# Kernel tuning notes

Hardware: AMD Instinct MI355X
Metric: run time of the kernel (lower is better)

The kernel has to match this reference:

```python
import jax, jax.numpy as jnp
import numpy as np

N = 4096          # number_of_node
DIN = 3           # dim_input (forced: fc1 expects N*dim_input == N*3 after last stage)
DOUT = 4          # dim_output
DACT = N          # dim_action defaults to number_of_node
B = 128


def setup_inputs() -> dict:
    key = jax.random.key(0)
    ks = jax.random.split(key, 12)
    X = jax.random.normal(ks[0], (B, N * DIN), dtype=jnp.float32)
    adj = jax.random.uniform(ks[1], (N, N), dtype=jnp.float32)
    def lin(kw, kb, fan_in, fan_out):
        bound = 1.0 / np.sqrt(fan_in)
        W = jax.random.uniform(kw, (fan_in, fan_out), minval=-bound, maxval=bound, dtype=jnp.float32)
        b = jax.random.uniform(kb, (fan_out,), minval=-bound, maxval=bound, dtype=jnp.float32)
        return W, b
    W1, b1 = lin(ks[2], ks[3], DIN, 4)
    W2, b2 = lin(ks[4], ks[5], 4, DOUT)
    W3, b3 = lin(ks[6], ks[7], DOUT, 3)
    Wfc, bfc = lin(ks[8], ks[9], N * DIN, 54)
    Wout, bout = lin(ks[10], ks[11], 54, DACT)
    return {"X": X, "adj": adj, "W1": W1, "b1": b1, "W2": W2, "b2": b2,
            "W3": W3, "b3": b3, "Wfc": Wfc, "bfc": bfc, "Wout": Wout, "bout": bout}


def reference(X, adj, W1, b1, W2, b2, W3, b3, Wfc, bfc, Wout, bout):
    # X: [B, N*DIN] -> [B, N, DIN]
    h = X.reshape(X.shape[0], N, DIN)
    # three (adj @ h) aggregations fused with tiny Linear + ReLU
    h = jax.nn.relu(jnp.einsum('nm,bmf->bnf', adj, h) @ W1 + b1)   # [B,N,4]
    h = jax.nn.relu(jnp.einsum('nm,bmf->bnf', adj, h) @ W2 + b2)   # [B,N,DOUT]
    h = jax.nn.relu(jnp.einsum('nm,bmf->bnf', adj, h) @ W3 + b3)   # [B,N,3]
    flat = h.reshape(h.shape[0], -1)                               # [B, N*3]
    hid = jax.nn.relu(flat @ Wfc + bfc)                            # [B, 54]
    q_value = hid @ Wout + bout                                    # [B, DACT]
    return q_value
```

## Files before the change

### kernel.cpp

```cpp
#include <hip/hip_runtime.h>


typedef __bf16 bf16x8 __attribute__((ext_vector_type(8)));
typedef float  f32x4  __attribute__((ext_vector_type(4)));

#define N_NODE 4096
#define BATCH  128

__global__ __launch_bounds__(256) void prep_k(const float* __restrict__ adj,
                                              __bf16* __restrict__ adjB,
                                              const float* __restrict__ X,
                                              const float* __restrict__ W1,
                                              __bf16* __restrict__ G0,
                                              float* __restrict__ hid_acc) {
    const int blk = blockIdx.x, tx = threadIdx.x;
    if (blk < 8192) {
        const int g = blk * 256 + tx;
        const int lane = g & 63, ka = (g >> 6) & 127, rb = g >> 13;
        const int row = rb * 16 + (lane & 15);
        const int kb  = ka * 32 + ((lane >> 4) & 3) * 8;
        const float4* s = (const float4*)(adj + (size_t)row * 4096 + kb);
        float4 u = s[0];
        float4 v = s[1];
        bf16x8 o = { (__bf16)u.x, (__bf16)u.y, (__bf16)u.z, (__bf16)u.w,
                     (__bf16)v.x, (__bf16)v.y, (__bf16)v.z, (__bf16)v.w };
        *(bf16x8*)(adjB + (size_t)g * 8) = o;
    } else if (blk < 9216) {
        const int g = (blk - 8192) * 256 + tx;
        const int lp = g & 63, cbg = (g >> 6) & 31, kc = g >> 11;
        const int c = cbg * 16 + (lp & 15);
        const int b = c >> 2, f = c & 3;
        const float w0 = W1[0 * 4 + f], w1 = W1[1 * 4 + f], w2 = W1[2 * 4 + f];
        const int mb = kc * 32 + ((lp >> 4) & 3) * 8;
        const float* Xb = X + (size_t)b * 12288 + (size_t)mb * 3;
        bf16x8 o;
#pragma unroll
        for (int j = 0; j < 8; ++j) {
            const float v = Xb[j * 3 + 0] * w0 + Xb[j * 3 + 1] * w1 + Xb[j * 3 + 2] * w2;
            o[j] = (__bf16)v;
        }
        *(bf16x8*)(G0 + (size_t)g * 8) = o;
    } else {
        const int i = (blk - 9216) * 256 + tx;
        if (i < BATCH * 54) hid_acc[i] = 0.f;
    }
}

template <int MODE>
__global__ __launch_bounds__(512, 4) void gcn_k(const __bf16* __restrict__ A,
                                                const __bf16* __restrict__ Bp,
                                                const float* __restrict__ Wa,
                                                const float* __restrict__ ba,
                                                const float* __restrict__ Wb,
                                                __bf16* __restrict__ Op,
                                                float* __restrict__ hidOut) {
    __shared__ __align__(16) unsigned char smem[49664];
    const int tx = threadIdx.x;
    const int wave = tx >> 6, lane = tx & 63;
    const int quad = lane >> 4, lr = lane & 15;

    const int l = blockIdx.x;
    const int xcd = l & 7, s = l >> 3;
    const int mi = xcd * 8 + (s & 7), ci = s >> 3;
    const int m0 = mi * 64;

    const __bf16* pA[4];
#pragma unroll
    for (int i = 0; i < 4; ++i)
        pA[i] = A + (size_t)(mi * 4 + i) * 65536 + wave * 512 + lane * 8;
    const __bf16* pB[4];
#pragma unroll
    for (int j = 0; j < 4; ++j)
        pB[j] = Bp + (size_t)(wave * 32 + (ci * 4 + j)) * 512 + lane * 8;

    f32x4 acc[4][4] = {};

#pragma unroll 4
    for (int kt = 0; kt < 16; ++kt) {
        bf16x8 af[4], bv[4];
#pragma unroll
        for (int i = 0; i < 4; ++i)
            af[i] = *(const bf16x8*)(pA[i] + kt * 4096);
#pragma unroll
        for (int j = 0; j < 4; ++j)
            bv[j] = *(const bf16x8*)(pB[j] + kt * 131072);
#pragma unroll
        for (int i = 0; i < 4; ++i)
#pragma unroll
            for (int j = 0; j < 4; ++j)
                acc[i][j] = __builtin_amdgcn_mfma_f32_16x16x32_bf16(
                    af[i], bv[j], acc[i][j], 0, 0, 0);
    }

    float* part = (float*)smem;
    float* Ct   = (float*)(smem + 32768);
#pragma unroll
    for (int r = 0; r < 4; ++r) {
        __syncthreads();
#pragma unroll
        for (int u = 0; u < 4; ++u)
            *(f32x4*)(part + (wave * 4 + u) * 256 + lane * 4) = acc[r][u];
        __syncthreads();
        if (wave < 4) {
            f32x4 fin = {};
#pragma unroll
            for (int sl = 0; sl < 8; ++sl)
                fin += *(const f32x4*)(part + (sl * 4 + wave) * 256 + lane * 4);
#pragma unroll
            for (int rr = 0; rr < 4; ++rr)
                Ct[(r * 16 + quad * 4 + rr) * 66 + wave * 16 + lr] = fin[rr];
        }
    }
    __syncthreads();

    if (MODE == 0) {
        const int g2 = tx;
        const int lp = g2 & 63, cbl = (g2 >> 6) & 3, kcl = g2 >> 8;
        const int cl = cbl * 16 + (lp & 15);
        const float bf = ba[cl & 3];
        const int mb = kcl * 32 + ((lp >> 4) & 3) * 8;
        bf16x8 o;
#pragma unroll
        for (int j = 0; j < 8; ++j)
            o[j] = (__bf16)fmaxf(Ct[(mb + j) * 66 + cl] + bf, 0.f);
        *(bf16x8*)(Op + ((size_t)((mi * 2 + kcl) * 32 + (ci * 4 + cbl)) * 64 + lp) * 8) = o;
    } else if (MODE == 1) {
        float W2l[16], W3l[12], bl2[4];
#pragma unroll
        for (int i = 0; i < 16; ++i) W2l[i] = Wa[i];
#pragma unroll
        for (int i = 0; i < 12; ++i) W3l[i] = Wb[i];
#pragma unroll
        for (int i = 0; i < 4; ++i) bl2[i] = ba[i];
        const int g2 = tx;
        const int lp = g2 & 63, cbl = (g2 >> 6) & 3, kcl = g2 >> 8;
        const int cl = cbl * 16 + (lp & 15);
        const int bloc = cl >> 2, f3 = cl & 3;
        const int mb = kcl * 32 + ((lp >> 4) & 3) * 8;
        bf16x8 o;
#pragma unroll
        for (int j = 0; j < 8; ++j) {
            const float* row = &Ct[(mb + j) * 66 + bloc * 4];
            float v = 0.f;
            if (f3 < 3) {
#pragma unroll
                for (int fo = 0; fo < 4; ++fo) {
                    const float tmp = fmaxf(row[0] * W2l[fo] + row[1] * W2l[4 + fo] +
                                            row[2] * W2l[8 + fo] + row[3] * W2l[12 + fo] +
                                            bl2[fo], 0.f);
                    const float w3a = W3l[fo * 3 + 0], w3b = W3l[fo * 3 + 1],
                                w3c = W3l[fo * 3 + 2];
                    v += tmp * (f3 == 0 ? w3a : (f3 == 1 ? w3b : w3c));
                }
            }
            o[j] = (__bf16)v;
        }
        *(bf16x8*)(Op + ((size_t)((mi * 2 + kcl) * 32 + (ci * 4 + cbl)) * 64 + lp) * 8) = o;
    } else {
        float* red = part;
        const float b30 = ba[0], b31 = ba[1], b32 = ba[2];
        float accf[16];
#pragma unroll
        for (int b = 0; b < 16; ++b) accf[b] = 0.f;
        if (lane < 54) {
            for (int nn = 0; nn < 8; ++nn) {
                const int n = wave * 8 + nn;
#pragma unroll
                for (int f = 0; f < 3; ++f) {
                    const float w = Wa[((size_t)(m0 + n) * 3 + f) * 54 + lane];
                    const float bf = (f == 0) ? b30 : (f == 1 ? b31 : b32);
#pragma unroll
                    for (int b = 0; b < 16; ++b) {
                        const float r = fmaxf(Ct[n * 66 + b * 4 + f] + bf, 0.f);
                        accf[b] += r * w;
                    }
                }
            }
        }
#pragma unroll
        for (int b = 0; b < 16; ++b)
            red[(wave * 16 + b) * 64 + lane] = accf[b];
        __syncthreads();
        if (wave == 0 && lane < 54) {
            for (int b = 0; b < 16; ++b) {
                float s2 = 0.f;
#pragma unroll
                for (int w8 = 0; w8 < 8; ++w8)
                    s2 += red[(w8 * 16 + b) * 64 + lane];
                atomicAdd(&hidOut[(ci * 16 + b) * 54 + lane], s2);
            }
        }
    }
}

__global__ __launch_bounds__(256) void fc2_k(const float* __restrict__ hid_acc,
                                             const float* __restrict__ bfc,
                                             const float* __restrict__ Wout,
                                             const float* __restrict__ bout,
                                             float* __restrict__ out) {
    const int tx = threadIdx.x;
    const int a  = blockIdx.x * 256 + tx;
    const int b0 = blockIdx.y * 4;
    __shared__ float hs[4 * 54];
    if (tx < 216) {
        const int j = tx % 54;
        hs[tx] = fmaxf(hid_acc[b0 * 54 + tx] + bfc[j], 0.f);
    }
    __syncthreads();
    float a0 = 0.f, a1 = 0.f, a2 = 0.f, a3 = 0.f;
    for (int j = 0; j < 54; ++j) {
        float w = Wout[(size_t)j * N_NODE + a];
        a0 += hs[0 * 54 + j] * w;
        a1 += hs[1 * 54 + j] * w;
        a2 += hs[2 * 54 + j] * w;
        a3 += hs[3 * 54 + j] * w;
    }
    float bo = bout[a];
    out[(size_t)(b0 + 0) * N_NODE + a] = a0 + bo;
    out[(size_t)(b0 + 1) * N_NODE + a] = a1 + bo;
    out[(size_t)(b0 + 2) * N_NODE + a] = a2 + bo;
    out[(size_t)(b0 + 3) * N_NODE + a] = a3 + bo;
}

extern "C" void kernel_launch(void* const* d_in, const int* in_sizes, int n_in,
                              void* d_out, int out_size, void* d_ws, size_t ws_size,
                              hipStream_t stream) {
    const float* X    = (const float*)d_in[0];
    const float* adj  = (const float*)d_in[1];
    const float* W1   = (const float*)d_in[2];
    const float* b1   = (const float*)d_in[3];
    const float* W2   = (const float*)d_in[4];
    const float* b2   = (const float*)d_in[5];
    const float* W3   = (const float*)d_in[6];
    const float* b3   = (const float*)d_in[7];
    const float* Wfc  = (const float*)d_in[8];
    const float* bfc  = (const float*)d_in[9];
    const float* Wout = (const float*)d_in[10];
    const float* bout = (const float*)d_in[11];
    float* out = (float*)d_out;

    char* w = (char*)d_ws;
    __bf16* adjB = (__bf16*)w;
    __bf16* G0   = (__bf16*)(w + 33554432);
    __bf16* H1   = (__bf16*)(w + 33554432 + 4194304);
    __bf16* H2g  = (__bf16*)(w + 33554432 + 2 * 4194304);
    float*  hid  = (float*)(w + 33554432 + 3 * 4194304);

    prep_k<<<9243, 256, 0, stream>>>(adj, adjB, X, W1, G0, hid);

    gcn_k<0><<<512, 512, 0, stream>>>(adjB, G0, nullptr, b1, nullptr, H1, nullptr);
    gcn_k<1><<<512, 512, 0, stream>>>(adjB, H1, W2, b2, W3, H2g, nullptr);
    gcn_k<2><<<512, 512, 0, stream>>>(adjB, H2g, Wfc, b3, nullptr, nullptr, hid);

    fc2_k<<<dim3(16, 32), 256, 0, stream>>>(hid, bfc, Wout, bout, out);
}
```

Measured before the change: 209.2 us.

## Double GCN block row tile to 128 with 1024-thread blocks

Each gcn block now covers 128 adjacency rows using 16 waves: two row groups of eight K-split waves each, with the launch reduced to 256 blocks. The split-K reduction and the per-mode epilogue run in two serialized halves over the same shared buffer. For MODE 2, the partial FC sums of the two row groups are merged in shared memory before the atomic add. The aim is more reuse of the B operand per block and fewer blocks. In exchange it adds extra barriers, leaves half the waves idle during the epilogues, and `launch_bounds(1024,4)` may push the compiler toward tight register limits.

```diff
diff --git a/kernel.cpp b/kernel.cpp
--- a/kernel.cpp
+++ b/kernel.cpp
@@ -47,31 +47,32 @@
 }
 
 template <int MODE>
-__global__ __launch_bounds__(512, 4) void gcn_k(const __bf16* __restrict__ A,
-                                                const __bf16* __restrict__ Bp,
-                                                const float* __restrict__ Wa,
-                                                const float* __restrict__ ba,
-                                                const float* __restrict__ Wb,
-                                                __bf16* __restrict__ Op,
-                                                float* __restrict__ hidOut) {
+__global__ __launch_bounds__(1024, 4) void gcn_k(const __bf16* __restrict__ A,
+                                                 const __bf16* __restrict__ Bp,
+                                                 const float* __restrict__ Wa,
+                                                 const float* __restrict__ ba,
+                                                 const float* __restrict__ Wb,
+                                                 __bf16* __restrict__ Op,
+                                                 float* __restrict__ hidOut) {
     __shared__ __align__(16) unsigned char smem[49664];
     const int tx = threadIdx.x;
     const int wave = tx >> 6, lane = tx & 63;
+    const int wm = wave >> 3, wk = wave & 7;
     const int quad = lane >> 4, lr = lane & 15;
 
     const int l = blockIdx.x;
     const int xcd = l & 7, s = l >> 3;
-    const int mi = xcd * 8 + (s & 7), ci = s >> 3;
-    const int m0 = mi * 64;
+    const int mi = xcd * 4 + (s & 3), ci = s >> 2;
+    const int m0 = mi * 128;
 
     const __bf16* pA[4];
 #pragma unroll
     for (int i = 0; i < 4; ++i)
-        pA[i] = A + (size_t)(mi * 4 + i) * 65536 + wave * 512 + lane * 8;
+        pA[i] = A + (size_t)(mi * 8 + wm * 4 + i) * 65536 + wk * 512 + lane * 8;
     const __bf16* pB[4];
 #pragma unroll
     for (int j = 0; j < 4; ++j)
-        pB[j] = Bp + (size_t)(wave * 32 + (ci * 4 + j)) * 512 + lane * 8;
+        pB[j] = Bp + (size_t)(wk * 32 + (ci * 4 + j)) * 512 + lane * 8;
 
     f32x4 acc[4][4] = {};
 
@@ -94,92 +95,124 @@
 
     float* part = (float*)smem;
     float* Ct   = (float*)(smem + 32768);
-#pragma unroll
-    for (int r = 0; r < 4; ++r) {
-        __syncthreads();
-#pragma unroll
-        for (int u = 0; u < 4; ++u)
-            *(f32x4*)(part + (wave * 4 + u) * 256 + lane * 4) = acc[r][u];
-        __syncthreads();
-        if (wave < 4) {
-            f32x4 fin = {};
-#pragma unroll
-            for (int sl = 0; sl < 8; ++sl)
-                fin += *(const f32x4*)(part + (sl * 4 + wave) * 256 + lane * 4);
-#pragma unroll
-            for (int rr = 0; rr < 4; ++rr)
-                Ct[(r * 16 + quad * 4 + rr) * 66 + wave * 16 + lr] = fin[rr];
-        }
-    }
-    __syncthreads();
-
-    if (MODE == 0) {
-        const int g2 = tx;
-        const int lp = g2 & 63, cbl = (g2 >> 6) & 3, kcl = g2 >> 8;
-        const int cl = cbl * 16 + (lp & 15);
-        const float bf = ba[cl & 3];
-        const int mb = kcl * 32 + ((lp >> 4) & 3) * 8;
-        bf16x8 o;
-#pragma unroll
-        for (int j = 0; j < 8; ++j)
-            o[j] = (__bf16)fmaxf(Ct[(mb + j) * 66 + cl] + bf, 0.f);
-        *(bf16x8*)(Op + ((size_t)((mi * 2 + kcl) * 32 + (ci * 4 + cbl)) * 64 + lp) * 8) = o;
-    } else if (MODE == 1) {
-        float W2l[16], W3l[12], bl2[4];
-#pragma unroll
-        for (int i = 0; i < 16; ++i) W2l[i] = Wa[i];
-#pragma unroll
-        for (int i = 0; i < 12; ++i) W3l[i] = Wb[i];
-#pragma unroll
-        for (int i = 0; i < 4; ++i) bl2[i] = ba[i];
-        const int g2 = tx;
-        const int lp = g2 & 63, cbl = (g2 >> 6) & 3, kcl = g2 >> 8;
-        const int cl = cbl * 16 + (lp & 15);
-        const int bloc = cl >> 2, f3 = cl & 3;
-        const int mb = kcl * 32 + ((lp >> 4) & 3) * 8;
-        bf16x8 o;
-#pragma unroll
-        for (int j = 0; j < 8; ++j) {
-            const float* row = &Ct[(mb + j) * 66 + bloc * 4];
-            float v = 0.f;
-            if (f3 < 3) {
-#pragma unroll
-                for (int fo = 0; fo < 4; ++fo) {
-                    const float tmp = fmaxf(row[0] * W2l[fo] + row[1] * W2l[4 + fo] +
-                                            row[2] * W2l[8 + fo] + row[3] * W2l[12 + fo] +
-                                            bl2[fo], 0.f);
-                    const float w3a = W3l[fo * 3 + 0], w3b = W3l[fo * 3 + 1],
-                                w3c = W3l[fo * 3 + 2];
-                    v += tmp * (f3 == 0 ? w3a : (f3 == 1 ? w3b : w3c));
+
+    float accf[16];
+    if (MODE == 2) {
+#pragma unroll
+        for (int b = 0; b < 16; ++b) accf[b] = 0.f;
+    }
+
+#pragma unroll 1
+    for (int h = 0; h < 2; ++h) {
+#pragma unroll
+        for (int r = 0; r < 4; ++r) {
+            __syncthreads();
+            if (wm == h) {
+#pragma unroll
+                for (int u = 0; u < 4; ++u)
+                    *(f32x4*)(part + (wk * 4 + u) * 256 + lane * 4) = acc[r][u];
+            }
+            __syncthreads();
+            if (wm == h && wk < 4) {
+                f32x4 fin = {};
+#pragma unroll
+                for (int sl = 0; sl < 8; ++sl)
+                    fin += *(const f32x4*)(part + (sl * 4 + wk) * 256 + lane * 4);
+#pragma unroll
+                for (int rr = 0; rr < 4; ++rr)
+                    Ct[(r * 16 + quad * 4 + rr) * 66 + wk * 16 + lr] = fin[rr];
+            }
+        }
+        __syncthreads();
+
+        if (MODE == 0) {
+            if (tx < 512) {
+                const int lp = tx & 63, cbl = (tx >> 6) & 3, kcl = tx >> 8;
+                const int cl = cbl * 16 + (lp & 15);
+                const float bf = ba[cl & 3];
+                const int mb = kcl * 32 + ((lp >> 4) & 3) * 8;
+                bf16x8 o;
+#pragma unroll
+                for (int j = 0; j < 8; ++j)
+                    o[j] = (__bf16)fmaxf(Ct[(mb + j) * 66 + cl] + bf, 0.f);
+                *(bf16x8*)(Op + ((size_t)((mi * 4 + h * 2 + kcl) * 32 +
+                                          (ci * 4 + cbl)) * 64 + lp) * 8) = o;
+            }
+        } else if (MODE == 1) {
+            if (tx < 512) {
+                float W2l[16], W3l[12], bl2[4];
+#pragma unroll
+                for (int i = 0; i < 16; ++i) W2l[i] = Wa[i];
+#pragma unroll
+                for (int i = 0; i < 12; ++i) W3l[i] = Wb[i];
+#pragma unroll
+                for (int i = 0; i < 4; ++i) bl2[i] = ba[i];
+                const int lp = tx & 63, cbl = (tx >> 6) & 3, kcl = tx >> 8;
+                const int cl = cbl * 16 + (lp & 15);
+                const int bloc = cl >> 2, f3 = cl & 3;
+                const int mb = kcl * 32 + ((lp >> 4) & 3) * 8;
+                bf16x8 o;
+#pragma unroll
+                for (int j = 0; j < 8; ++j) {
+                    const float* row = &Ct[(mb + j) * 66 + bloc * 4];
+                    float v = 0.f;
+                    if (f3 < 3) {
+#pragma unroll
+                        for (int fo = 0; fo < 4; ++fo) {
+                            const float tmp = fmaxf(row[0] * W2l[fo] + row[1] * W2l[4 + fo] +
+                                                    row[2] * W2l[8 + fo] + row[3] * W2l[12 + fo] +
+                                                    bl2[fo], 0.f);
+                            const float w3a = W3l[fo * 3 + 0], w3b = W3l[fo * 3 + 1],
+                                        w3c = W3l[fo * 3 + 2];
+                            v += tmp * (f3 == 0 ? w3a : (f3 == 1 ? w3b : w3c));
+                        }
+                    }
+                    o[j] = (__bf16)v;
                 }
-            }
-            o[j] = (__bf16)v;
-        }
-        *(bf16x8*)(Op + ((size_t)((mi * 2 + kcl) * 32 + (ci * 4 + cbl)) * 64 + lp) * 8) = o;
-    } else {
-        float* red = part;
-        const float b30 = ba[0], b31 = ba[1], b32 = ba[2];
-        float accf[16];
-#pragma unroll
-        for (int b = 0; b < 16; ++b) accf[b] = 0.f;
-        if (lane < 54) {
-            for (int nn = 0; nn < 8; ++nn) {
-                const int n = wave * 8 + nn;
-#pragma unroll
-                for (int f = 0; f < 3; ++f) {
-                    const float w = Wa[((size_t)(m0 + n) * 3 + f) * 54 + lane];
-                    const float bf = (f == 0) ? b30 : (f == 1 ? b31 : b32);
-#pragma unroll
-                    for (int b = 0; b < 16; ++b) {
-                        const float r = fmaxf(Ct[n * 66 + b * 4 + f] + bf, 0.f);
-                        accf[b] += r * w;
+                *(bf16x8*)(Op + ((size_t)((mi * 4 + h * 2 + kcl) * 32 +
+                                          (ci * 4 + cbl)) * 64 + lp) * 8) = o;
+            }
+        } else {
+            const float b30 = ba[0], b31 = ba[1], b32 = ba[2];
+            if (lane < 54) {
+                for (int nn = 0; nn < 4; ++nn) {
+                    const int nl = wave * 4 + nn;
+                    const int ng = m0 + h * 64 + nl;
+#pragma unroll
+                    for (int f = 0; f < 3; ++f) {
+                        const float w = Wa[((size_t)ng * 3 + f) * 54 + lane];
+                        const float bf = (f == 0) ? b30 : (f == 1 ? b31 : b32);
+#pragma unroll
+                        for (int b = 0; b < 16; ++b) {
+                            const float r = fmaxf(Ct[nl * 66 + b * 4 + f] + bf, 0.f);
+                            accf[b] += r * w;
+                        }
                     }
                 }
             }
         }
-#pragma unroll
-        for (int b = 0; b < 16; ++b)
-            red[(wave * 16 + b) * 64 + lane] = accf[b];
+    }
+
+    if (MODE == 2) {
+        float* red = part;
+        __syncthreads();
+        if (wave >= 8) {
+#pragma unroll
+            for (int b = 0; b < 16; ++b)
+                red[((wave - 8) * 16 + b) * 64 + lane] = accf[b];
+        }
+        __syncthreads();
+        if (wave < 8) {
+#pragma unroll
+            for (int b = 0; b < 16; ++b)
+                accf[b] += red[(wave * 16 + b) * 64 + lane];
+        }
+        __syncthreads();
+        if (wave < 8) {
+#pragma unroll
+            for (int b = 0; b < 16; ++b)
+                red[(wave * 16 + b) * 64 + lane] = accf[b];
+        }
         __syncthreads();
         if (wave == 0 && lane < 54) {
             for (int b = 0; b < 16; ++b) {
@@ -248,9 +281,9 @@
 
     prep_k<<<9243, 256, 0, stream>>>(adj, adjB, X, W1, G0, hid);
 
-    gcn_k<0><<<512, 512, 0, stream>>>(adjB, G0, nullptr, b1, nullptr, H1, nullptr);
-    gcn_k<1><<<512, 512, 0, stream>>>(adjB, H1, W2, b2, W3, H2g, nullptr);
-    gcn_k<2><<<512, 512, 0, stream>>>(adjB, H2g, Wfc, b3, nullptr, nullptr, hid);
+    gcn_k<0><<<256, 1024, 0, stream>>>(adjB, G0, nullptr, b1, nullptr, H1, nullptr);
+    gcn_k<1><<<256, 1024, 0, stream>>>(adjB, H1, W2, b2, W3, H2g, nullptr);
+    gcn_k<2><<<256, 1024, 0, stream>>>(adjB, H2g, Wfc, b3, nullptr, nullptr, hid);
 
     fc2_k<<<dim3(16, 32), 256, 0, stream>>>(hid, bfc, Wout, bout, out);
 }
```

Result: slower. 251.6 us (+20.3%).
